# Optimization experiments

Hardware: AMD Instinct MI355X
Metric: run time of the kernel (lower is better)

Reference implementation:

```python
import jax, jax.numpy as jnp
import numpy as np

ALPHA = 0.2  # LeakyReLU slope
S1, S2 = 5, 10  # neighbor sample sizes, hard-coded in the torch forward

N, F, D, C, B = 100000, 512, 256, 40, 16384


def setup_inputs() -> dict:
    key = jax.random.key(0)
    ks = jax.random.split(key, 7)
    x = jax.random.normal(ks[0], (N, F), dtype=jnp.float32)
    # xavier-like scaling for the weights
    W1 = jax.random.normal(ks[1], (D, F), dtype=jnp.float32) * (2.0 / (D + F)) ** 0.5
    W2 = jax.random.normal(ks[2], (D, D), dtype=jnp.float32) * (2.0 / (D + D)) ** 0.5
    Wc = jax.random.normal(ks[3], (C, D), dtype=jnp.float32) * (2.0 / (C + D)) ** 0.5
    nodes = jax.random.randint(ks[4], (B,), 0, N, dtype=jnp.int32)
    neigh1 = jax.random.randint(ks[5], (N, S1), 0, N, dtype=jnp.int32)
    neigh2 = jax.random.randint(ks[6], (B, S2), 0, N, dtype=jnp.int32)
    return {"x": x, "W1": W1, "W2": W2, "Wc": Wc,
            "nodes": nodes, "neigh1": neigh1, "neigh2": neigh2}


def leaky_relu(v):
    return jnp.where(v >= 0, v, ALPHA * v)


def reference(x, W1, W2, Wc, nodes, neigh1, neigh2):
    # Layer 1 (MeanAggregator, gcn=True): mean over sampled neighbors + self,
    # then linear transform + LeakyReLU. Computed for all N nodes.
    agg1 = (x[neigh1].sum(axis=1) + x) / (S1 + 1)          # [N, F]
    h1 = leaky_relu(agg1 @ W1.T)                            # [N, D]
    # Layer 2: mean over sampled neighbors + self, on batch nodes.
    agg2 = (h1[neigh2].sum(axis=1) + h1[nodes]) / (S2 + 1)  # [B, D]
    h2 = leaky_relu(agg2 @ W2.T)                            # [B, D]
    # scores = self.weight.mm(x_2.t()).t()
    scores = h2 @ Wc.T                                      # [B, C]
    return scores
```

## Files before the change

### kernel.cpp

```cpp
#include <hip/hip_runtime.h>
#include <hip/hip_bf16.h>


#define NN 100000
#define FF 512
#define DD 256
#define BB 16384
#define CC 40

typedef __attribute__((ext_vector_type(8))) short bf16x8;
typedef __attribute__((ext_vector_type(4))) float f32x4;
typedef unsigned short u16;
typedef unsigned int u32;
typedef __attribute__((ext_vector_type(4))) u32 u32x4;

__device__ __forceinline__ float bf_lo(u32 u) { u32 v = u << 16; float f; __builtin_memcpy(&f, &v, 4); return f; }
__device__ __forceinline__ float bf_hi(u32 u) { u32 v = u & 0xffff0000u; float f; __builtin_memcpy(&f, &v, 4); return f; }
__device__ __forceinline__ float2 bf2f(u32 u) { return make_float2(bf_lo(u), bf_hi(u)); }
__device__ __forceinline__ float asf(u32 u) { float f; __builtin_memcpy(&f, &u, 4); return f; }
__device__ __forceinline__ u32 packbf2(float a, float b) {
  __hip_bfloat162 h = __float22bfloat162_rn(make_float2(a, b));
  u32 u; __builtin_memcpy(&u, &h, 4); return u;
}
__device__ __forceinline__ u16 fbits(float v) {
  __hip_bfloat16 h = __float2bfloat16(v);
  u16 u; __builtin_memcpy(&u, &h, 2); return u;
}
__device__ __forceinline__ float lrelu(float v) { return v >= 0.f ? v : 0.2f * v; }
__device__ __forceinline__ int swz(int r, int c) { return r * 128 + ((c ^ (r & 7)) << 4); }
__device__ __forceinline__ void gld_lds16(const u16* g, void* l) {
  __builtin_amdgcn_global_load_lds((const __attribute__((address_space(1))) unsigned int*)g,
                                   (__attribute__((address_space(3))) unsigned int*)l, 16, 0, 0);
}
__device__ __forceinline__ u32x4 ld4(const float* p) { return *(const u32x4*)p; }

__global__ __launch_bounds__(256) void k0_cvt(
    const float* __restrict__ W1, const float* __restrict__ W2, const float* __restrict__ Wc,
    u16* __restrict__ w1b, u16* __restrict__ w2b, u16* __restrict__ wcb,
    u32* __restrict__ flagw)
{
  const int i = blockIdx.x * 256 + threadIdx.x;
  if (i < 25024) flagw[i] = 0;
  if (i < 16384) {
    const int r = i >> 6, cc = i & 63;
    const int lc = (cc & ~3) | ((cc ^ r) & 3);
    const float* s = W1 + (u32)r * 512 + (u32)lc * 8;
    const float4 v0 = *(const float4*)s;
    const float4 v1 = *(const float4*)(s + 4);
    uint4 o;
    o.x = packbf2(v0.x, v0.y); o.y = packbf2(v0.z, v0.w);
    o.z = packbf2(v1.x, v1.y); o.w = packbf2(v1.z, v1.w);
    *(uint4*)(w1b + (u32)r * 512 + (u32)cc * 8) = o;
    return;
  }
  const float* src; u16* dst; int r, cc;
  if (i < 24576)      { int j = i - 16384; src = W2; dst = w2b; r = j >> 5; cc = j & 31; }
  else if (i < 25856) { int j = i - 24576; src = Wc; dst = wcb; r = j >> 5; cc = j & 31; }
  else return;
  const int g = cc >> 3, cp = cc & 7;
  const float* s = src + (u32)r * 256 + g * 64 + (u32)(cp ^ (r & 7)) * 8;
  const float4 v0 = *(const float4*)s;
  const float4 v1 = *(const float4*)(s + 4);
  uint4 o;
  o.x = packbf2(v0.x, v0.y); o.y = packbf2(v0.z, v0.w);
  o.z = packbf2(v1.x, v1.y); o.w = packbf2(v1.z, v1.w);
  *(uint4*)(dst + (u32)r * 256 + g * 64 + cp * 8) = o;
}

__global__ __launch_bounds__(256) void k0b_flags(
    const int* __restrict__ nodes, const int* __restrict__ neigh2,
    unsigned char* __restrict__ flags)
{
  const int i = blockIdx.x * 256 + threadIdx.x;
  int idx;
  if (i < BB) idx = nodes[i];
  else if (i < BB + BB * 10) idx = neigh2[i - BB];
  else return;
  flags[idx] = 1;
}

__global__ __launch_bounds__(256, 4) void k1_gemm(
    const float* __restrict__ x, const u16* __restrict__ w1b, u16* __restrict__ z)
{
  __shared__ __align__(16) unsigned char lds[32768];

  const int t = threadIdx.x;
  const int rowBase = blockIdx.x * 64;
  const int lane = t & 63, w = t >> 6;
  const int lr = lane & 15, kg = lane >> 4;

  int rw = rowBase + w * 16 + lr; if (rw > NN - 1) rw = NN - 1;
  const float* xr = x + (u32)rw * FF + (u32)kg * 8;

  const u32 bofs = (u32)(w * 16 + (lane >> 2)) * FF + (u32)(lane & 3) * 8;

  const int bvb = lr * 64 + ((kg ^ (lr & 3)) << 4);

  f32x4 acc[16];
#pragma unroll
  for (int n = 0; n < 16; ++n) acc[n] = (f32x4)0.0f;

  u32x4 pa[2];
  pa[0] = ld4(xr);
  pa[1] = ld4(xr + 4);
#pragma unroll
  for (int i = 0; i < 4; ++i)
    gld_lds16(w1b + bofs + (u32)i * 64 * FF, lds + w * 1024 + i * 4096);
#pragma unroll
  for (int i = 0; i < 4; ++i)
    gld_lds16(w1b + bofs + (u32)i * 64 * FF + 32, lds + 16384 + w * 1024 + i * 4096);

#pragma unroll 2
  for (int ks = 0; ks < 16; ++ks) {
    bf16x8 av;
    {
      u32x4 p;
      p[0] = packbf2(asf(pa[0][0]), asf(pa[0][1]));
      p[1] = packbf2(asf(pa[0][2]), asf(pa[0][3]));
      p[2] = packbf2(asf(pa[1][0]), asf(pa[1][1]));
      p[3] = packbf2(asf(pa[1][2]), asf(pa[1][3]));
      av = *(bf16x8*)&p;
    }
    if (ks < 15) {
      pa[0] = ld4(xr + (u32)(ks + 1) * 32);
      pa[1] = ld4(xr + (u32)(ks + 1) * 32 + 4);
      asm volatile("s_waitcnt vmcnt(6)" ::: "memory");
    } else {
      asm volatile("s_waitcnt vmcnt(0)" ::: "memory");
    }
    __builtin_amdgcn_sched_barrier(0);
    __builtin_amdgcn_s_barrier();
    __builtin_amdgcn_sched_barrier(0);

    const int bo = (ks & 1) * 16384;
#pragma unroll
    for (int n = 0; n < 16; ++n) {
      const bf16x8 bv = *(const bf16x8*)(lds + bo + bvb + n * 1024);
      acc[n] = __builtin_amdgcn_mfma_f32_16x16x32_bf16(bv, av, acc[n], 0, 0, 0);
    }
    __builtin_amdgcn_sched_barrier(0);
    __builtin_amdgcn_s_barrier();
    __builtin_amdgcn_sched_barrier(0);
    if (ks <= 13) {
      unsigned char* bl = lds + bo + w * 1024;
#pragma unroll
      for (int i = 0; i < 4; ++i)
        gld_lds16(w1b + bofs + (u32)i * 64 * FF + (u32)(ks + 2) * 32, bl + i * 4096);
    }
  }

  __syncthreads();
  {
    const int zr = w * 16 + lr;
#pragma unroll
    for (int n = 0; n < 16; ++n) {
      const int zc = n * 16 + kg * 4;
      uint2 o;
      o.x = packbf2(acc[n][0], acc[n][1]);
      o.y = packbf2(acc[n][2], acc[n][3]);
      const int ch = zc >> 3;
      const int pch = (ch & 24) | ((ch ^ (zr & 7)) & 7);
      *(uint2*)(lds + zr * 512 + pch * 16 + (zc & 7) * 2) = o;
    }
  }
  __syncthreads();
#pragma unroll
  for (int i = 0; i < 8; ++i) {
    const int id = t + i * 256;
    const int rr = id >> 5, cc = id & 31;
    const int pch = (cc & 24) | ((cc ^ (rr & 7)) & 7);
    const uint4 v = *(const uint4*)(lds + rr * 512 + pch * 16);
    *(uint4*)(z + (u32)(rowBase + rr) * DD + cc * 8) = v;
  }
}

__global__ __launch_bounds__(256) void k2_agg1(
    const u16* __restrict__ z, const int* __restrict__ neigh1, u16* __restrict__ h1,
    const unsigned char* __restrict__ flags)
{
  const int t = threadIdx.x;
  const int row = blockIdx.x * 8 + (t >> 5);
  if (!flags[row]) return;
  const int ch = t & 31;
  const u32 o0 = (u32)row * DD + ch * 8;
  uint4 a = *(const uint4*)(z + o0);
  float2 s0 = bf2f(a.x), s1 = bf2f(a.y), s2 = bf2f(a.z), s3 = bf2f(a.w);
#pragma unroll
  for (int j = 0; j < 5; ++j) {
    const int idx = neigh1[row * 5 + j];
    const uint4 v = *(const uint4*)(z + (u32)idx * DD + ch * 8);
    s0.x += bf_lo(v.x); s0.y += bf_hi(v.x);
    s1.x += bf_lo(v.y); s1.y += bf_hi(v.y);
    s2.x += bf_lo(v.z); s2.y += bf_hi(v.z);
    s3.x += bf_lo(v.w); s3.y += bf_hi(v.w);
  }
  const float sc = 1.0f / 6.0f;
  uint4 o;
  o.x = packbf2(lrelu(s0.x * sc), lrelu(s0.y * sc));
  o.y = packbf2(lrelu(s1.x * sc), lrelu(s1.y * sc));
  o.z = packbf2(lrelu(s2.x * sc), lrelu(s2.y * sc));
  o.w = packbf2(lrelu(s3.x * sc), lrelu(s3.y * sc));
  *(uint4*)(h1 + o0) = o;
}

__global__ __launch_bounds__(512, 2) void k3_fused(
    const u16* __restrict__ h1, const u16* __restrict__ w2b, const u16* __restrict__ wcb,
    const int* __restrict__ nodes, const int* __restrict__ neigh2, float* __restrict__ out)
{
  __shared__ __align__(16) unsigned char lds[65536];

  const int t = threadIdx.x;
  const int rowBase = blockIdx.x * 64;
  const int lane = t & 63, w = t >> 6;
  const int wm = w >> 2, wn = w & 3;
  const int lr = lane & 15, kg = lane >> 4;

#pragma unroll
  for (int i = 0; i < 3; ++i) {
    const int id = t + i * 512;
    uint4 v = make_uint4(0u, 0u, 0u, 0u);
    if (id < 1280) v = *(const uint4*)(wcb + (u32)id * 8);
    *(uint4*)(lds + 40960 + id * 16) = v;
  }

  const int r = t >> 3, c = t & 7;
  const int b = rowBase + r;
  u32 offA[11];
  offA[0] = (u32)nodes[b] * DD + (u32)c * 8;
#pragma unroll
  for (int j = 0; j < 10; ++j)
    offA[1 + j] = (u32)neigh2[b * 10 + j] * DD + (u32)c * 8;
  const int aW = swz(r, c);

  const u32 bofs = (u32)(w * 8 + (lane >> 3)) * DD + (u32)(lane & 7) * 8;
  unsigned char* bl0 = lds + 8192 + w * 1024;

  int aA[2][2], bA[2][4];
#pragma unroll
  for (int kk = 0; kk < 2; ++kk) {
    const int cb = kk * 4 + kg;
#pragma unroll
    for (int m = 0; m < 2; ++m) aA[kk][m] = swz(wm * 32 + m * 16 + lr, cb);
#pragma unroll
    for (int n = 0; n < 4; ++n) bA[kk][n] = 8192 + swz(wn * 64 + n * 16 + lr, cb);
  }

  f32x4 acc[2][4];
#pragma unroll
  for (int m = 0; m < 2; ++m)
#pragma unroll
    for (int n = 0; n < 4; ++n) acc[m][n] = (f32x4)0.0f;

  uint4 ag[11];
#pragma unroll
  for (int j = 0; j < 11; ++j) ag[j] = *(const uint4*)(h1 + offA[j]);

  for (int ks = 0; ks < 4; ++ks) {
    if (ks) __builtin_amdgcn_s_barrier();
    {
      float2 s0 = make_float2(0.f, 0.f), s1 = make_float2(0.f, 0.f);
      float2 s2 = make_float2(0.f, 0.f), s3 = make_float2(0.f, 0.f);
#pragma unroll
      for (int j = 0; j < 11; ++j) {
        s0.x += bf_lo(ag[j].x); s0.y += bf_hi(ag[j].x);
        s1.x += bf_lo(ag[j].y); s1.y += bf_hi(ag[j].y);
        s2.x += bf_lo(ag[j].z); s2.y += bf_hi(ag[j].z);
        s3.x += bf_lo(ag[j].w); s3.y += bf_hi(ag[j].w);
      }
      const float sc = 1.0f / 11.0f;
      uint4 o;
      o.x = packbf2(s0.x * sc, s0.y * sc);
      o.y = packbf2(s1.x * sc, s1.y * sc);
      o.z = packbf2(s2.x * sc, s2.y * sc);
      o.w = packbf2(s3.x * sc, s3.y * sc);
      *(uint4*)(lds + aW) = o;
    }
#pragma unroll
    for (int i = 0; i < 4; ++i)
      gld_lds16(w2b + bofs + (u32)i * 64 * DD + (u32)ks * 64, bl0 + i * 8192);
    __syncthreads();
    if (ks < 3) {
#pragma unroll
      for (int j = 0; j < 11; ++j)
        ag[j] = *(const uint4*)(h1 + offA[j] + (u32)(ks + 1) * 64);
    }
    __builtin_amdgcn_sched_barrier(0);
#pragma unroll
    for (int kk = 0; kk < 2; ++kk) {
      bf16x8 av[2], bv[4];
#pragma unroll
      for (int m = 0; m < 2; ++m) av[m] = *(const bf16x8*)(lds + aA[kk][m]);
#pragma unroll
      for (int n = 0; n < 4; ++n) bv[n] = *(const bf16x8*)(lds + bA[kk][n]);
#pragma unroll
      for (int m = 0; m < 2; ++m)
#pragma unroll
        for (int n = 0; n < 4; ++n)
          acc[m][n] = __builtin_amdgcn_mfma_f32_16x16x32_bf16(av[m], bv[n], acc[m][n], 0, 0, 0);
    }
  }

  __syncthreads();
#pragma unroll
  for (int m = 0; m < 2; ++m) {
#pragma unroll
    for (int j = 0; j < 4; ++j) {
      const int row = wm * 32 + m * 16 + kg * 4 + j;
#pragma unroll
      for (int n = 0; n < 4; ++n) {
        const int col = wn * 64 + n * 16 + lr;
        const int ch = col >> 3;
        const int pch = (ch & 24) | ((ch ^ row) & 7);
        *(u16*)(lds + row * 512 + pch * 16 + (col & 7) * 2) = fbits(lrelu(acc[m][n][j]));
      }
    }
  }
  __syncthreads();

  if (w < 4) {
    f32x4 acc2[3];
#pragma unroll
    for (int n = 0; n < 3; ++n) acc2[n] = (f32x4)0.0f;
    const int arow = w * 16 + lr;
#pragma unroll
    for (int ks2 = 0; ks2 < 8; ++ks2) {
      const int chb = ks2 * 4 + kg;
      const int pchA = (chb & 24) | ((chb ^ arow) & 7);
      const bf16x8 a = *(const bf16x8*)(lds + arow * 512 + pchA * 16);
#pragma unroll
      for (int n = 0; n < 3; ++n) {
        const int brow = n * 16 + lr;
        const int pchB = (chb & 24) | ((chb ^ brow) & 7);
        const bf16x8 bb = *(const bf16x8*)(lds + 40960 + brow * 512 + pchB * 16);
        acc2[n] = __builtin_amdgcn_mfma_f32_16x16x32_bf16(a, bb, acc2[n], 0, 0, 0);
      }
    }
#pragma unroll
    for (int n = 0; n < 3; ++n) {
      const int col = n * 16 + lr;
      if (col < CC) {
#pragma unroll
        for (int j = 0; j < 4; ++j) {
          const int rr = rowBase + w * 16 + kg * 4 + j;
          out[(u32)rr * CC + col] = acc2[n][j];
        }
      }
    }
  }
}

extern "C" void kernel_launch(void* const* d_in, const int* in_sizes, int n_in,
                              void* d_out, int out_size, void* d_ws, size_t ws_size,
                              hipStream_t stream) {
  const float* x    = (const float*)d_in[0];
  const float* W1   = (const float*)d_in[1];
  const float* W2   = (const float*)d_in[2];
  const float* Wc   = (const float*)d_in[3];
  const int* nodes  = (const int*)d_in[4];
  const int* neigh1 = (const int*)d_in[5];
  const int* neigh2 = (const int*)d_in[6];

  u16* z   = (u16*)d_ws;
  u16* h1  = z + (size_t)100096 * 256;
  u16* w1b = h1 + (size_t)100096 * 256;
  u16* w2b = w1b + (size_t)256 * 512;
  u16* wcb = w2b + (size_t)256 * 256;
  u32* flagw = (u32*)(wcb + (size_t)40 * 256);
  unsigned char* flags = (unsigned char*)flagw;

  k0_cvt<<<dim3(101), dim3(256), 0, stream>>>(W1, W2, Wc, w1b, w2b, wcb, flagw);
  k0b_flags<<<dim3(704), dim3(256), 0, stream>>>(nodes, neigh2, flags);
  k1_gemm<<<dim3(1563), dim3(256), 0, stream>>>(x, w1b, z);
  k2_agg1<<<dim3(12500), dim3(256), 0, stream>>>(z, neigh1, h1, flags);
  k3_fused<<<dim3(256), dim3(512), 0, stream>>>(h1, w2b, wcb, nodes, neigh2, (float*)d_out);
}
```

Measured before the change: 155.4 us.

## Enlarge GEMM block to 128 rows with triple-buffered LDS and deeper prefetch

Result: faster. 139.9 us (-10.0%).

```diff
diff --git a/kernel.cpp b/kernel.cpp
--- a/kernel.cpp
+++ b/kernel.cpp
@@ -43,7 +43,7 @@
   if (i < 25024) flagw[i] = 0;
   if (i < 16384) {
     const int r = i >> 6, cc = i & 63;
-    const int lc = (cc & ~3) | ((cc ^ r) & 3);
+    const int lc = (cc & ~3) | ((cc ^ r ^ (r >> 2)) & 3);
     const float* s = W1 + (u32)r * 512 + (u32)lc * 8;
     const float4 v0 = *(const float4*)s;
     const float4 v1 = *(const float4*)(s + 4);
@@ -79,74 +79,75 @@
   flags[idx] = 1;
 }
 
-__global__ __launch_bounds__(256, 4) void k1_gemm(
+__global__ __launch_bounds__(512, 4) void k1_gemm(
     const float* __restrict__ x, const u16* __restrict__ w1b, u16* __restrict__ z)
 {
-  __shared__ __align__(16) unsigned char lds[32768];
+  __shared__ __align__(16) unsigned char lds[65536];
 
   const int t = threadIdx.x;
-  const int rowBase = blockIdx.x * 64;
+  const int rowBase = blockIdx.x * 128;
   const int lane = t & 63, w = t >> 6;
   const int lr = lane & 15, kg = lane >> 4;
 
   int rw = rowBase + w * 16 + lr; if (rw > NN - 1) rw = NN - 1;
   const float* xr = x + (u32)rw * FF + (u32)kg * 8;
 
-  const u32 bofs = (u32)(w * 16 + (lane >> 2)) * FF + (u32)(lane & 3) * 8;
-
-  const int bvb = lr * 64 + ((kg ^ (lr & 3)) << 4);
+  const u32 bofs = (u32)(w * 32 + (lane >> 2)) * FF + (u32)(lane & 3) * 8;
+
+  const int pch = (kg ^ (lr & 3) ^ ((lr >> 2) & 3)) & 3;
+  const int bvb = lr * 64 + (pch << 4);
 
   f32x4 acc[16];
 #pragma unroll
   for (int n = 0; n < 16; ++n) acc[n] = (f32x4)0.0f;
 
-  u32x4 pa[2];
-  pa[0] = ld4(xr);
-  pa[1] = ld4(xr + 4);
-#pragma unroll
-  for (int i = 0; i < 4; ++i)
-    gld_lds16(w1b + bofs + (u32)i * 64 * FF, lds + w * 1024 + i * 4096);
-#pragma unroll
-  for (int i = 0; i < 4; ++i)
-    gld_lds16(w1b + bofs + (u32)i * 64 * FF + 32, lds + 16384 + w * 1024 + i * 4096);
-
-#pragma unroll 2
+  u32x4 pa[2][2];
+  pa[0][0] = ld4(xr);       pa[0][1] = ld4(xr + 4);
+  gld_lds16(w1b + bofs,           lds + w * 2048);
+  gld_lds16(w1b + bofs + 16 * FF, lds + w * 2048 + 1024);
+  pa[1][0] = ld4(xr + 32);  pa[1][1] = ld4(xr + 32 + 4);
+  gld_lds16(w1b + bofs + 32,           lds + 16384 + w * 2048);
+  gld_lds16(w1b + bofs + 16 * FF + 32, lds + 16384 + w * 2048 + 1024);
+
+#pragma unroll
   for (int ks = 0; ks < 16; ++ks) {
+    const int p = ks & 1;
     bf16x8 av;
     {
-      u32x4 p;
-      p[0] = packbf2(asf(pa[0][0]), asf(pa[0][1]));
-      p[1] = packbf2(asf(pa[0][2]), asf(pa[0][3]));
-      p[2] = packbf2(asf(pa[1][0]), asf(pa[1][1]));
-      p[3] = packbf2(asf(pa[1][2]), asf(pa[1][3]));
-      av = *(bf16x8*)&p;
-    }
-    if (ks < 15) {
-      pa[0] = ld4(xr + (u32)(ks + 1) * 32);
-      pa[1] = ld4(xr + (u32)(ks + 1) * 32 + 4);
+      u32x4 q;
+      q[0] = packbf2(asf(pa[p][0][0]), asf(pa[p][0][1]));
+      q[1] = packbf2(asf(pa[p][0][2]), asf(pa[p][0][3]));
+      q[2] = packbf2(asf(pa[p][1][0]), asf(pa[p][1][1]));
+      q[3] = packbf2(asf(pa[p][1][2]), asf(pa[p][1][3]));
+      av = *(bf16x8*)&q;
+    }
+    if (ks <= 13) {
+      pa[p][0] = ld4(xr + (u32)(ks + 2) * 32);
+      pa[p][1] = ld4(xr + (u32)(ks + 2) * 32 + 4);
       asm volatile("s_waitcnt vmcnt(6)" ::: "memory");
+    } else if (ks == 14) {
+      asm volatile("s_waitcnt vmcnt(4)" ::: "memory");
     } else {
       asm volatile("s_waitcnt vmcnt(0)" ::: "memory");
-    }
-    __builtin_amdgcn_sched_barrier(0);
-    __builtin_amdgcn_s_barrier();
-    __builtin_amdgcn_sched_barrier(0);
-
-    const int bo = (ks & 1) * 16384;
-#pragma unroll
-    for (int n = 0; n < 16; ++n) {
-      const bf16x8 bv = *(const bf16x8*)(lds + bo + bvb + n * 1024);
-      acc[n] = __builtin_amdgcn_mfma_f32_16x16x32_bf16(bv, av, acc[n], 0, 0, 0);
     }
     __builtin_amdgcn_sched_barrier(0);
     __builtin_amdgcn_s_barrier();
     __builtin_amdgcn_sched_barrier(0);
     if (ks <= 13) {
-      unsigned char* bl = lds + bo + w * 1024;
-#pragma unroll
-      for (int i = 0; i < 4; ++i)
-        gld_lds16(w1b + bofs + (u32)i * 64 * FF + (u32)(ks + 2) * 32, bl + i * 4096);
-    }
+      unsigned char* bl = lds + ((ks + 2) % 3) * 16384 + w * 2048;
+      gld_lds16(w1b + bofs + (u32)(ks + 2) * 32,           bl);
+      gld_lds16(w1b + bofs + 16 * FF + (u32)(ks + 2) * 32, bl + 1024);
+    }
+    __builtin_amdgcn_sched_barrier(0);
+
+    const unsigned char* bp = lds + (ks % 3) * 16384;
+    __builtin_amdgcn_s_setprio(1);
+#pragma unroll
+    for (int n = 0; n < 16; ++n) {
+      const bf16x8 bv = *(const bf16x8*)(bp + n * 1024 + bvb);
+      acc[n] = __builtin_amdgcn_mfma_f32_16x16x32_bf16(bv, av, acc[n], 0, 0, 0);
+    }
+    __builtin_amdgcn_s_setprio(0);
   }
 
   __syncthreads();
@@ -159,17 +160,17 @@
       o.x = packbf2(acc[n][0], acc[n][1]);
       o.y = packbf2(acc[n][2], acc[n][3]);
       const int ch = zc >> 3;
-      const int pch = (ch & 24) | ((ch ^ (zr & 7)) & 7);
-      *(uint2*)(lds + zr * 512 + pch * 16 + (zc & 7) * 2) = o;
+      const int pc8 = (ch & 24) | ((ch ^ (zr & 7)) & 7);
+      *(uint2*)(lds + zr * 512 + pc8 * 16 + (zc & 7) * 2) = o;
     }
   }
   __syncthreads();
 #pragma unroll
   for (int i = 0; i < 8; ++i) {
-    const int id = t + i * 256;
+    const int id = t + i * 512;
     const int rr = id >> 5, cc = id & 31;
-    const int pch = (cc & 24) | ((cc ^ (rr & 7)) & 7);
-    const uint4 v = *(const uint4*)(lds + rr * 512 + pch * 16);
+    const int pc8 = (cc & 24) | ((cc ^ (rr & 7)) & 7);
+    const uint4 v = *(const uint4*)(lds + rr * 512 + pc8 * 16);
     *(uint4*)(z + (u32)(rowBase + rr) * DD + cc * 8) = v;
   }
 }
@@ -370,7 +371,7 @@
 
   k0_cvt<<<dim3(101), dim3(256), 0, stream>>>(W1, W2, Wc, w1b, w2b, wcb, flagw);
   k0b_flags<<<dim3(704), dim3(256), 0, stream>>>(nodes, neigh2, flags);
-  k1_gemm<<<dim3(1563), dim3(256), 0, stream>>>(x, w1b, z);
+  k1_gemm<<<dim3(782), dim3(512), 0, stream>>>(x, w1b, z);
   k2_agg1<<<dim3(12500), dim3(256), 0, stream>>>(z, neigh1, h1, flags);
   k3_fused<<<dim3(256), dim3(512), 0, stream>>>(h1, w2b, wcb, nodes, neigh2, (float*)d_out);
 }
```
